# Kernel optimization log

Hardware: AMD Instinct MI355X
Metric: run time of the kernel (lower is better)

Reference implementation:

```python
import jax, jax.numpy as jnp
import numpy as np

B, T, EMB, NDIM = 8, 2048, 1024, 1024


def setup_inputs() -> dict:
    key = jax.random.key(0)
    k1, k2, k3, k4 = jax.random.split(key, 4)
    X = jax.random.normal(k1, (B, T, EMB), dtype=jnp.float32)
    # Linear(emb, ndim, bias=False); stored as [emb, ndim] so projection is X @ W.
    scale = 1.0 / np.sqrt(EMB)
    Wq = jax.random.normal(k2, (EMB, NDIM), dtype=jnp.float32) * scale
    Wk = jax.random.normal(k3, (EMB, NDIM), dtype=jnp.float32) * scale
    Wv = jax.random.normal(k4, (EMB, NDIM), dtype=jnp.float32) * scale
    return {"X": X, "Wq": Wq, "Wk": Wk, "Wv": Wv}


def reference(X, Wq, Wk, Wv):
    ndim = Wq.shape[-1]
    T_ = X.shape[1]
    Q = X @ Wq  # [B,T,ndim]
    K = X @ Wk  # [B,T,ndim]
    V = X @ Wv  # [B,T,ndim]
    # scores[b,t,s] = Q[b,t] . K[b,s], scaled by ndim^-0.5
    scores = jnp.einsum("btd,bsd->bts", Q, K) * (ndim ** -0.5)
    mask = jnp.tril(jnp.ones((T_, T_), dtype=bool))  # causal lower-triangular
    scores = jnp.where(mask, scores, -jnp.inf)
    # NOTE: source uses F.softmax(..., dim=1) -> normalize over the QUERY axis
    # (columns of the [T,T] matrix), not the usual key axis. Replicated faithfully.
    probs = jax.nn.softmax(scores, axis=1)
    # dropout is identity in eval / p=0 deterministic baseline
    return probs @ V  # [B,T,ndim]
```

## Files before the change

kernel.cpp:

```cpp
#include <hip/hip_runtime.h>
#include <hip/hip_bf16.h>

#define B_   8
#define T_   2048
#define EMB_ 1024
#define ND_  1024
#define NTB  16
#define NPAIR 136

typedef __attribute__((ext_vector_type(8))) short   bf8_t;
typedef __attribute__((ext_vector_type(4))) float   f32x4;

__device__ __forceinline__ unsigned short f2bf(float f) {
  union { float f; unsigned int u; } c; c.f = f;
  unsigned int u = c.u;
  unsigned int r = (u + 0x7FFFu + ((u >> 16) & 1u)) >> 16;
  return (unsigned short)r;
}

__device__ __forceinline__ float bf2f(unsigned short b) {
  union { unsigned int u; float f; } c; c.u = ((unsigned int)b) << 16;
  return c.f;
}

__device__ __forceinline__ void gload_lds16(const unsigned short* g, unsigned short* l) {
  __builtin_amdgcn_global_load_lds(
      (const __attribute__((address_space(1))) unsigned int*)g,
      (__attribute__((address_space(3))) unsigned int*)l,
      16, 0, 0);
}

__device__ __forceinline__ void stage128x32(const unsigned short* __restrict__ g,
                                            int lda, unsigned short* lds,
                                            int wave, int lane) {
  const int rsub = lane >> 2;
  const int koff = (lane & 3) * 8;
#pragma unroll
  for (int c = 0; c < 2; ++c) {
    const int chunk = wave * 2 + c;
    const unsigned short* src = g + (size_t)(chunk * 16 + rsub) * lda + koff;
    gload_lds16(src, lds + chunk * 512);
  }
}

__device__ __forceinline__ void mfma_step(const unsigned short* As, const unsigned short* Bs,
                                          f32x4 acc[4][4], int lane, int wm, int wn) {
  const int r = lane & 15, k8 = (lane >> 4) * 8;
  bf8_t a[4], b[4];
#pragma unroll
  for (int m = 0; m < 4; ++m)
    a[m] = *(const bf8_t*)(As + (size_t)(wm * 64 + m * 16 + r) * 32 + k8);
#pragma unroll
  for (int n = 0; n < 4; ++n)
    b[n] = *(const bf8_t*)(Bs + (size_t)(wn * 64 + n * 16 + r) * 32 + k8);
#pragma unroll
  for (int m = 0; m < 4; ++m)
#pragma unroll
    for (int n = 0; n < 4; ++n)
      acc[m][n] = __builtin_amdgcn_mfma_f32_16x16x32_bf16(a[m], b[n], acc[m][n], 0, 0, 0);
}

__device__ __forceinline__ void zero_acc(f32x4 acc[4][4]) {
#pragma unroll
  for (int m = 0; m < 4; ++m)
#pragma unroll
    for (int n = 0; n < 4; ++n)
#pragma unroll
      for (int q = 0; q < 4; ++q) acc[m][n][q] = 0.f;
}

__device__ __forceinline__ void tri_decode(int p, int& tblk, int& sblk) {
  int t = (int)((sqrtf(8.0f * (float)p + 1.0f) - 1.0f) * 0.5f);
  while ((t + 1) * (t + 2) / 2 <= p) ++t;
  while (t * (t + 1) / 2 > p) --t;
  tblk = t;
  sblk = p - t * (t + 1) / 2;
}

__global__ void __launch_bounds__(256) cvt_x_kernel(const float* __restrict__ in,
                                                    unsigned short* __restrict__ out) {
  const int i = (blockIdx.x * 256 + threadIdx.x) * 4;
  float4 v = *(const float4*)(in + i);
  ushort4 o = make_ushort4(f2bf(v.x), f2bf(v.y), f2bf(v.z), f2bf(v.w));
  *(ushort4*)(out + i) = o;
}

__global__ void __launch_bounds__(256) transpose_w_kernel(const float* __restrict__ W,
                                                          unsigned short* __restrict__ Wt,
                                                          float cscale) {
  __shared__ unsigned short tile[32][33];
  const int n0 = blockIdx.x * 32, k0 = blockIdx.y * 32;
  const int tx = threadIdx.x & 31, ty = threadIdx.x >> 5;
#pragma unroll
  for (int r = 0; r < 32; r += 8) {
    float v = W[(size_t)(k0 + ty + r) * ND_ + n0 + tx];
    tile[tx][ty + r] = f2bf(v * cscale);
  }
  __syncthreads();
#pragma unroll
  for (int r = 0; r < 32; r += 8) {
    Wt[(size_t)(n0 + ty + r) * EMB_ + k0 + tx] = tile[ty + r][tx];
  }
}


#define LDSA(d, h) (lds256 + ((d) * 2 + (h)) * 8192)
#define LDSB(d, h) (lds256 + 32768 + ((d) * 2 + (h)) * 8192)
#define SB0() __builtin_amdgcn_sched_barrier(0)
#define BAR() __builtin_amdgcn_s_barrier()

__device__ __forceinline__ void stage_half(const unsigned short* __restrict__ g, int lda,
                                           unsigned short* lhalf, int wave, int lane) {
  const int r3 = lane >> 3, c3 = lane & 7;
  const int colsw = ((c3 ^ r3) << 3);
#pragma unroll
  for (int j = 0; j < 2; ++j) {
    const int row = wave * 8 + r3 + 64 * j;
    gload_lds16(g + (size_t)row * lda + colsw, lhalf + wave * 512 + j * 4096);
  }
}

__device__ __forceinline__ bf8_t read_frag(const unsigned short* half, int r, int ks, int lane) {
  const int col = (((ks) << 5) + ((lane >> 4) << 3)) ^ ((r & 7) << 3);
  return *(const bf8_t*)(half + r * 64 + col);
}

#define MFMA_QUAD(MB, AF, AOFF) do { \
  __builtin_amdgcn_s_setprio(1); \
  _Pragma("unroll") \
  for (int mi = 0; mi < 2; ++mi) \
    _Pragma("unroll") \
    for (int nf = 0; nf < 4; ++nf) \
      _Pragma("unroll") \
      for (int ks = 0; ks < 2; ++ks) \
        acc[(MB) * 2 + mi][nf] = __builtin_amdgcn_mfma_f32_16x16x32_bf16( \
            (AF)[(AOFF) + mi][ks], bfr[nf][ks], acc[(MB) * 2 + mi][nf], 0, 0, 0); \
  __builtin_amdgcn_s_setprio(0); \
} while (0)

template <int OUTMODE>
__global__ void __launch_bounds__(512, 2)
gemm_xw256_kernel(const unsigned short* __restrict__ A,
                  const unsigned short* __restrict__ Bt,
                  unsigned short* __restrict__ C) {
  extern __shared__ unsigned short lds256[];
  const int tid = threadIdx.x, lane = tid & 63, wave = tid >> 6;
  const int wm = wave >> 2, wn = wave & 3;
  const int m0 = blockIdx.y * 256, n0 = blockIdx.x * 256;
  const unsigned short* Ab = A + (size_t)m0 * EMB_;
  const unsigned short* Bb = Bt + (size_t)n0 * EMB_;

  f32x4 acc[8][4];
#pragma unroll
  for (int i = 0; i < 8; ++i)
#pragma unroll
    for (int j = 0; j < 4; ++j)
#pragma unroll
      for (int q = 0; q < 4; ++q) acc[i][j][q] = 0.f;

  const int arow = lane & 15;
  const int brow = (wn & 1) * 64 + (lane & 15);

  stage_half(Ab,                            EMB_, LDSA(0, 0), wave, lane);
  stage_half(Ab + (size_t)128 * EMB_,       EMB_, LDSA(0, 1), wave, lane);
  stage_half(Bb,                            EMB_, LDSB(0, 0), wave, lane);
  stage_half(Bb + (size_t)128 * EMB_,       EMB_, LDSB(0, 1), wave, lane);
  stage_half(Bb + 64,                       EMB_, LDSB(1, 0), wave, lane);
  stage_half(Bb + (size_t)128 * EMB_ + 64,  EMB_, LDSB(1, 1), wave, lane);
  stage_half(Ab + 64,                       EMB_, LDSA(1, 0), wave, lane);
  asm volatile("s_waitcnt vmcnt(6)" ::: "memory");
  SB0(); BAR(); SB0();

  for (int t = 0; t < 16; ++t) {
    const int d = t & 1;
    const unsigned short* Ah = LDSA(d, wm);
    const unsigned short* Bh = LDSB(d, wn >> 1);

    bf8_t bfr[4][2], af[4][2];
#pragma unroll
    for (int nf = 0; nf < 4; ++nf)
#pragma unroll
      for (int ks = 0; ks < 2; ++ks) bfr[nf][ks] = read_frag(Bh, brow + nf * 16, ks, lane);
#pragma unroll
    for (int mf = 0; mf < 4; ++mf)
#pragma unroll
      for (int ks = 0; ks < 2; ++ks) af[mf][ks] = read_frag(Ah, arow + mf * 16, ks, lane);
    SB0();
    if (t < 15) stage_half(Ab + (size_t)128 * EMB_ + (size_t)(t + 1) * 64, EMB_, LDSA(d ^ 1, 1), wave, lane);
    SB0(); BAR(); SB0();
    MFMA_QUAD(0, af, 0);
    SB0();
    asm volatile("s_waitcnt lgkmcnt(0)" ::: "memory");
    SB0(); BAR(); SB0();

    if (t < 14) stage_half(Bb + (size_t)(t + 2) * 64, EMB_, LDSB(d, 0), wave, lane);
    SB0(); BAR(); SB0();
    MFMA_QUAD(1, af, 2);
    SB0(); BAR(); SB0();

    bf8_t af2[4][2];
#pragma unroll
    for (int mf = 0; mf < 4; ++mf)
#pragma unroll
      for (int ks = 0; ks < 2; ++ks) af2[mf][ks] = read_frag(Ah, arow + (mf + 4) * 16, ks, lane);
    SB0();
    if (t < 14) stage_half(Bb + (size_t)128 * EMB_ + (size_t)(t + 2) * 64, EMB_, LDSB(d, 1), wave, lane);
    SB0(); BAR(); SB0();
    MFMA_QUAD(2, af2, 0);
    SB0();
    asm volatile("s_waitcnt lgkmcnt(0)" ::: "memory");
    SB0(); BAR(); SB0();

    if (t < 14) stage_half(Ab + (size_t)(t + 2) * 64, EMB_, LDSA(d, 0), wave, lane);
    if (t < 14)      { asm volatile("s_waitcnt vmcnt(6)" ::: "memory"); }
    else if (t == 14){ asm volatile("s_waitcnt vmcnt(0)" ::: "memory"); }
    SB0(); BAR(); SB0();
    MFMA_QUAD(3, af2, 2);
    SB0(); BAR(); SB0();
  }

  const int cc = lane & 15, cr4 = (lane >> 4) << 2;
#pragma unroll
  for (int mf = 0; mf < 8; ++mf)
#pragma unroll
    for (int nf = 0; nf < 4; ++nf)
#pragma unroll
      for (int q = 0; q < 4; ++q) {
        const int row = m0 + wm * 128 + mf * 16 + cr4 + q;
        const int col = n0 + wn * 64 + nf * 16 + cc;
        const unsigned short val = f2bf(acc[mf][nf][q]);
        if (OUTMODE == 0) {
          C[(size_t)row * ND_ + col] = val;
        } else {
          const int bb = row >> 11, tt = row & 2047;
          C[((size_t)bb * ND_ + col) * T_ + tt] = val;
        }
      }
}

__global__ void __launch_bounds__(256) scoretile_kernel(const unsigned short* __restrict__ Qb,
                                                        const unsigned short* __restrict__ Kb,
                                                        unsigned short* __restrict__ Sb,
                                                        float* __restrict__ pm,
                                                        float* __restrict__ pl) {
  int tblk, sblk;
  tri_decode(blockIdx.x, tblk, sblk);
  const int b = blockIdx.y;
  __shared__ unsigned short As[128 * 32], Bs[128 * 32];
  __shared__ float redm[2][2][4][16], redl[2][2][4][16];
  const int tid = threadIdx.x, lane = tid & 63, wave = tid >> 6;
  const int wm = wave >> 1, wn = wave & 1;
  const int t0 = tblk * 128, s0 = sblk * 128;
  const unsigned short* Qbase = Qb + ((size_t)b * T_ + t0) * ND_;
  const unsigned short* Kbase = Kb + ((size_t)b * T_ + s0) * ND_;
  f32x4 acc[4][4];
  zero_acc(acc);
  for (int k = 0; k < ND_; k += 32) {
    __syncthreads();
    stage128x32(Qbase + k, ND_, As, wave, lane);
    stage128x32(Kbase + k, ND_, Bs, wave, lane);
    __syncthreads();
    mfma_step(As, Bs, acc, lane, wm, wn);
  }
  const int cr = ((lane >> 4) << 2), cc = lane & 15;
  unsigned short* Pbase = Sb + (size_t)b * T_ * T_;
  const bool diag = (tblk == sblk);
  float rm[4], rl[4];
#pragma unroll
  for (int n = 0; n < 4; ++n) { rm[n] = -1e30f; rl[n] = 0.f; }
#pragma unroll
  for (int n = 0; n < 4; ++n) {
    const int s = s0 + wn * 64 + n * 16 + cc;
#pragma unroll
    for (int m = 0; m < 4; ++m)
#pragma unroll
      for (int q = 0; q < 4; ++q) {
        const int t = t0 + wm * 64 + m * 16 + cr + q;
        if (!diag || t >= s) {
          const unsigned short bv = f2bf(acc[m][n][q]);
          Pbase[(size_t)t * T_ + s] = bv;
          const float v = bf2f(bv);
          const float mm = fmaxf(rm[n], v);
          rl[n] = rl[n] * __expf(rm[n] - mm) + __expf(v - mm);
          rm[n] = mm;
        }
      }
  }
#pragma unroll
  for (int n = 0; n < 4; ++n) {
#pragma unroll
    for (int off = 16; off < 64; off <<= 1) {
      const float om = __shfl_xor(rm[n], off);
      const float ol = __shfl_xor(rl[n], off);
      const float mm = fmaxf(rm[n], om);
      rl[n] = rl[n] * __expf(rm[n] - mm) + ol * __expf(om - mm);
      rm[n] = mm;
    }
  }
  __syncthreads();
  if (lane < 16) {
#pragma unroll
    for (int n = 0; n < 4; ++n) { redm[wm][wn][n][lane] = rm[n]; redl[wm][wn][n][lane] = rl[n]; }
  }
  __syncthreads();
  if (wm == 0 && lane < 16) {
    const size_t base = (((size_t)b * NTB + sblk) * NTB + tblk) * 128;
#pragma unroll
    for (int n = 0; n < 4; ++n) {
      const float m0v = redm[0][wn][n][lane], l0v = redl[0][wn][n][lane];
      const float m1v = redm[1][wn][n][lane], l1v = redl[1][wn][n][lane];
      const float mm = fmaxf(m0v, m1v);
      const float ll = l0v * __expf(m0v - mm) + l1v * __expf(m1v - mm);
      pm[base + wn * 64 + n * 16 + lane] = mm;
      pl[base + wn * 64 + n * 16 + lane] = ll;
    }
  }
}

__global__ void __launch_bounds__(128) colreduce_kernel(const float* __restrict__ pm,
                                                        const float* __restrict__ pl,
                                                        float* __restrict__ colmax,
                                                        float* __restrict__ colinv) {
  const int sblk = blockIdx.x, b = blockIdx.y, c = threadIdx.x;
  float m = -1e30f, l = 0.f;
  for (int tblk = sblk; tblk < NTB; ++tblk) {
    const size_t base = (((size_t)b * NTB + sblk) * NTB + tblk) * 128;
    const float om = pm[base + c], ol = pl[base + c];
    const float mm = fmaxf(m, om);
    l = l * __expf(m - mm) + ol * __expf(om - mm);
    m = mm;
  }
  colmax[(size_t)b * T_ + sblk * 128 + c] = m;
  colinv[(size_t)b * T_ + sblk * 128 + c] = 1.0f / l;
}

__global__ void __launch_bounds__(256) pscale_kernel(unsigned short* __restrict__ Pb,
                                                     const float* __restrict__ colmax,
                                                     const float* __restrict__ colinv) {
  int tblk, sblk;
  tri_decode(blockIdx.x, tblk, sblk);
  const int b = blockIdx.y;
  const int s0 = sblk * 128, t0 = tblk * 128;
  const int tid = threadIdx.x;
  const int col8 = (tid & 15) * 8;
  const int rbase = tid >> 4;
  unsigned short* Pbase = Pb + (size_t)b * T_ * T_;
  float ms[8], inv[8];
#pragma unroll
  for (int j = 0; j < 8; ++j) {
    ms[j]  = colmax[(size_t)b * T_ + s0 + col8 + j];
    inv[j] = colinv[(size_t)b * T_ + s0 + col8 + j];
  }
  const bool diag = (tblk == sblk);
  for (int r = rbase; r < 128; r += 16) {
    const int t = t0 + r;
    unsigned short* p = Pbase + (size_t)t * T_ + s0 + col8;
    bf8_t v = *(bf8_t*)p;
#pragma unroll
    for (int j = 0; j < 8; ++j) {
      float pv = 0.f;
      if (!diag || t >= s0 + col8 + j) {
        pv = __expf(bf2f((unsigned short)v[j]) - ms[j]) * inv[j];
      }
      v[j] = (short)f2bf(pv);
    }
    *(bf8_t*)p = v;
  }
}

__global__ void __launch_bounds__(256) gemm_pv_kernel(const unsigned short* __restrict__ Pb,
                                                      const unsigned short* __restrict__ Vt,
                                                      float* __restrict__ out) {
  __shared__ unsigned short As[128 * 32], Bs[128 * 32];
  const int nblk = blockIdx.x, tblk = blockIdx.y, b = blockIdx.z;
  const int tid = threadIdx.x, lane = tid & 63, wave = tid >> 6;
  const int wm = wave >> 1, wn = wave & 1;
  const int m0 = tblk * 128, n0 = nblk * 128;
  const unsigned short* Ab = Pb + (size_t)b * T_ * T_ + (size_t)m0 * T_;
  const unsigned short* Bb = Vt + (size_t)b * ND_ * T_ + (size_t)n0 * T_;
  f32x4 acc[4][4];
  zero_acc(acc);
  const int kmax = m0 + 128;
  for (int k = 0; k < kmax; k += 32) {
    __syncthreads();
    stage128x32(Ab + k, T_, As, wave, lane);
    stage128x32(Bb + k, T_, Bs, wave, lane);
    __syncthreads();
    mfma_step(As, Bs, acc, lane, wm, wn);
  }
  float* Cb = out + (size_t)b * T_ * ND_;
  const int cr = ((lane >> 4) << 2), cc = lane & 15;
#pragma unroll
  for (int m = 0; m < 4; ++m)
#pragma unroll
    for (int n = 0; n < 4; ++n)
#pragma unroll
      for (int q = 0; q < 4; ++q) {
        const int row = m0 + wm * 64 + m * 16 + cr + q;
        const int col = n0 + wn * 64 + n * 16 + cc;
        Cb[(size_t)row * ND_ + col] = acc[m][n][q];
      }
}

extern "C" void kernel_launch(void* const* d_in, const int* in_sizes, int n_in,
                              void* d_out, int out_size, void* d_ws, size_t ws_size,
                              hipStream_t stream) {
  const float* X  = (const float*)d_in[0];
  const float* Wq = (const float*)d_in[1];
  const float* Wk = (const float*)d_in[2];
  const float* Wv = (const float*)d_in[3];
  float* out = (float*)d_out;
  (void)in_sizes; (void)n_in; (void)out_size;

  char* ws = (char*)d_ws;
  size_t off = 0;
  auto alloc = [&](size_t bytes) {
    void* p = ws + off;
    off += (bytes + 255) & ~(size_t)255;
    return p;
  };
  unsigned short* Xb  = (unsigned short*)alloc((size_t)B_ * T_ * EMB_ * 2);
  unsigned short* Wtq = (unsigned short*)alloc((size_t)ND_ * EMB_ * 2);
  unsigned short* Wtk = (unsigned short*)alloc((size_t)ND_ * EMB_ * 2);
  unsigned short* Wtv = (unsigned short*)alloc((size_t)ND_ * EMB_ * 2);
  unsigned short* Qb  = (unsigned short*)alloc((size_t)B_ * T_ * ND_ * 2);
  unsigned short* Kb  = (unsigned short*)alloc((size_t)B_ * T_ * ND_ * 2);
  unsigned short* Vt  = (unsigned short*)alloc((size_t)B_ * ND_ * T_ * 2);
  float* colmax = (float*)alloc((size_t)B_ * T_ * 4);
  float* colinv = (float*)alloc((size_t)B_ * T_ * 4);
  float* pm     = (float*)alloc((size_t)B_ * NTB * NTB * 128 * 4);
  float* pl     = (float*)alloc((size_t)B_ * NTB * NTB * 128 * 4);
  unsigned short* Pb  = (unsigned short*)alloc((size_t)B_ * T_ * T_ * 2);
  if (off > ws_size) return;

  hipFuncSetAttribute((const void*)&gemm_xw256_kernel<0>,
                      hipFuncAttributeMaxDynamicSharedMemorySize, 131072);
  hipFuncSetAttribute((const void*)&gemm_xw256_kernel<1>,
                      hipFuncAttributeMaxDynamicSharedMemorySize, 131072);

  hipLaunchKernelGGL(cvt_x_kernel, dim3((B_ * T_ * EMB_) / 1024), dim3(256), 0, stream, X, Xb);
  hipLaunchKernelGGL(transpose_w_kernel, dim3(32, 32), dim3(256), 0, stream, Wq, Wtq, 0.03125f);
  hipLaunchKernelGGL(transpose_w_kernel, dim3(32, 32), dim3(256), 0, stream, Wk, Wtk, 1.0f);
  hipLaunchKernelGGL(transpose_w_kernel, dim3(32, 32), dim3(256), 0, stream, Wv, Wtv, 1.0f);
  hipLaunchKernelGGL((gemm_xw256_kernel<0>), dim3(ND_ / 256, (B_ * T_) / 256), dim3(512), 131072, stream, Xb, Wtq, Qb);
  hipLaunchKernelGGL((gemm_xw256_kernel<0>), dim3(ND_ / 256, (B_ * T_) / 256), dim3(512), 131072, stream, Xb, Wtk, Kb);
  hipLaunchKernelGGL((gemm_xw256_kernel<1>), dim3(ND_ / 256, (B_ * T_) / 256), dim3(512), 131072, stream, Xb, Wtv, Vt);
  hipLaunchKernelGGL(scoretile_kernel, dim3(NPAIR, B_), dim3(256), 0, stream, Qb, Kb, Pb, pm, pl);
  hipLaunchKernelGGL(colreduce_kernel, dim3(NTB, B_), dim3(128), 0, stream, pm, pl, colmax, colinv);
  hipLaunchKernelGGL(pscale_kernel, dim3(NPAIR, B_), dim3(256), 0, stream, Pb, colmax, colinv);
  hipLaunchKernelGGL(gemm_pv_kernel, dim3(ND_ / 128, T_ / 128, B_), dim3(256), 0, stream, Pb, Vt, out);
}
```

Baseline: 328.1 us.

## Move score and PV GEMMs onto 256-tile pipelined MFMA path with balanced pairing

Replaces the simple 128x128 score-tile and PV GEMM kernels with versions built on the tuned 256-wide, 8-wave, double-buffered, swizzled-LDS pipeline already used for the projections. The score kernel now covers 256x256 causal tiles (36 pairs per batch) and writes explicit zeros above the diagonal. The PV kernel gives each block two row blocks, tb and 15-tb, so every block does a similar amount of causal work. The intent is higher MFMA utilisation and less per-tile load overhead, at the cost of more masked work on diagonal tiles and fewer, larger blocks.

New measurement: 305.2 us. -7.0%, faster.

```diff
diff --git a/kernel.cpp b/kernel.cpp
--- a/kernel.cpp
+++ b/kernel.cpp
@@ -7,6 +7,8 @@
 #define ND_  1024
 #define NTB  16
 #define NPAIR 136
+#define NTB2 8
+#define NPAIR2 36
 
 typedef __attribute__((ext_vector_type(8))) short   bf8_t;
 typedef __attribute__((ext_vector_type(4))) float   f32x4;
@@ -28,45 +30,6 @@
       (const __attribute__((address_space(1))) unsigned int*)g,
       (__attribute__((address_space(3))) unsigned int*)l,
       16, 0, 0);
-}
-
-__device__ __forceinline__ void stage128x32(const unsigned short* __restrict__ g,
-                                            int lda, unsigned short* lds,
-                                            int wave, int lane) {
-  const int rsub = lane >> 2;
-  const int koff = (lane & 3) * 8;
-#pragma unroll
-  for (int c = 0; c < 2; ++c) {
-    const int chunk = wave * 2 + c;
-    const unsigned short* src = g + (size_t)(chunk * 16 + rsub) * lda + koff;
-    gload_lds16(src, lds + chunk * 512);
-  }
-}
-
-__device__ __forceinline__ void mfma_step(const unsigned short* As, const unsigned short* Bs,
-                                          f32x4 acc[4][4], int lane, int wm, int wn) {
-  const int r = lane & 15, k8 = (lane >> 4) * 8;
-  bf8_t a[4], b[4];
-#pragma unroll
-  for (int m = 0; m < 4; ++m)
-    a[m] = *(const bf8_t*)(As + (size_t)(wm * 64 + m * 16 + r) * 32 + k8);
-#pragma unroll
-  for (int n = 0; n < 4; ++n)
-    b[n] = *(const bf8_t*)(Bs + (size_t)(wn * 64 + n * 16 + r) * 32 + k8);
-#pragma unroll
-  for (int m = 0; m < 4; ++m)
-#pragma unroll
-    for (int n = 0; n < 4; ++n)
-      acc[m][n] = __builtin_amdgcn_mfma_f32_16x16x32_bf16(a[m], b[n], acc[m][n], 0, 0, 0);
-}
-
-__device__ __forceinline__ void zero_acc(f32x4 acc[4][4]) {
-#pragma unroll
-  for (int m = 0; m < 4; ++m)
-#pragma unroll
-    for (int n = 0; n < 4; ++n)
-#pragma unroll
-      for (int q = 0; q < 4; ++q) acc[m][n][q] = 0.f;
 }
 
 __device__ __forceinline__ void tri_decode(int p, int& tblk, int& sblk) {
@@ -77,6 +40,25 @@
   sblk = p - t * (t + 1) / 2;
 }
 
+#define SB0() __builtin_amdgcn_sched_barrier(0)
+#define BAR() __builtin_amdgcn_s_barrier()
+
+__device__ __forceinline__ void stage_half(const unsigned short* __restrict__ g, int lda,
+                                           unsigned short* lhalf, int wave, int lane) {
+  const int r3 = lane >> 3, c3 = lane & 7;
+  const int colsw = ((c3 ^ r3) << 3);
+#pragma unroll
+  for (int j = 0; j < 2; ++j) {
+    const int row = wave * 8 + r3 + 64 * j;
+    gload_lds16(g + (size_t)row * lda + colsw, lhalf + wave * 512 + j * 4096);
+  }
+}
+
+__device__ __forceinline__ bf8_t read_frag(const unsigned short* half, int r, int ks, int lane) {
+  const int col = (((ks) << 5) + ((lane >> 4) << 3)) ^ ((r & 7) << 3);
+  return *(const bf8_t*)(half + r * 64 + col);
+}
+
 __global__ void __launch_bounds__(256) cvt_x_kernel(const float* __restrict__ in,
                                                     unsigned short* __restrict__ out) {
   const int i = (blockIdx.x * 256 + threadIdx.x) * 4;
@@ -103,27 +85,8 @@
   }
 }
 
-
 #define LDSA(d, h) (lds256 + ((d) * 2 + (h)) * 8192)
 #define LDSB(d, h) (lds256 + 32768 + ((d) * 2 + (h)) * 8192)
-#define SB0() __builtin_amdgcn_sched_barrier(0)
-#define BAR() __builtin_amdgcn_s_barrier()
-
-__device__ __forceinline__ void stage_half(const unsigned short* __restrict__ g, int lda,
-                                           unsigned short* lhalf, int wave, int lane) {
-  const int r3 = lane >> 3, c3 = lane & 7;
-  const int colsw = ((c3 ^ r3) << 3);
-#pragma unroll
-  for (int j = 0; j < 2; ++j) {
-    const int row = wave * 8 + r3 + 64 * j;
-    gload_lds16(g + (size_t)row * lda + colsw, lhalf + wave * 512 + j * 4096);
-  }
-}
-
-__device__ __forceinline__ bf8_t read_frag(const unsigned short* half, int r, int ks, int lane) {
-  const int col = (((ks) << 5) + ((lane >> 4) << 3)) ^ ((r & 7) << 3);
-  return *(const bf8_t*)(half + r * 64 + col);
-}
 
 #define MFMA_QUAD(MB, AF, AOFF) do { \
   __builtin_amdgcn_s_setprio(1); \
@@ -138,6 +101,60 @@
   __builtin_amdgcn_s_setprio(0); \
 } while (0)
 
+#define GEMM256_LOOP(ABASE, BBASE, LDK) \
+  stage_half((ABASE),                           (LDK), LDSA(0, 0), wave, lane); \
+  stage_half((ABASE) + (size_t)128 * (LDK),     (LDK), LDSA(0, 1), wave, lane); \
+  stage_half((BBASE),                           (LDK), LDSB(0, 0), wave, lane); \
+  stage_half((BBASE) + (size_t)128 * (LDK),     (LDK), LDSB(0, 1), wave, lane); \
+  stage_half((BBASE) + 64,                      (LDK), LDSB(1, 0), wave, lane); \
+  stage_half((BBASE) + (size_t)128 * (LDK) + 64,(LDK), LDSB(1, 1), wave, lane); \
+  stage_half((ABASE) + 64,                      (LDK), LDSA(1, 0), wave, lane); \
+  asm volatile("s_waitcnt vmcnt(6)" ::: "memory"); \
+  SB0(); BAR(); SB0(); \
+  for (int t = 0; t < 16; ++t) { \
+    const int d = t & 1; \
+    const unsigned short* Ah = LDSA(d, wm); \
+    const unsigned short* Bh = LDSB(d, wn >> 1); \
+    bf8_t bfr[4][2], af[4][2]; \
+    _Pragma("unroll") \
+    for (int nf = 0; nf < 4; ++nf) \
+      _Pragma("unroll") \
+      for (int ks = 0; ks < 2; ++ks) bfr[nf][ks] = read_frag(Bh, brow + nf * 16, ks, lane); \
+    _Pragma("unroll") \
+    for (int mf = 0; mf < 4; ++mf) \
+      _Pragma("unroll") \
+      for (int ks = 0; ks < 2; ++ks) af[mf][ks] = read_frag(Ah, arow + mf * 16, ks, lane); \
+    SB0(); \
+    if (t < 15) stage_half((ABASE) + (size_t)128 * (LDK) + (size_t)(t + 1) * 64, (LDK), LDSA(d ^ 1, 1), wave, lane); \
+    SB0(); BAR(); SB0(); \
+    MFMA_QUAD(0, af, 0); \
+    SB0(); \
+    asm volatile("s_waitcnt lgkmcnt(0)" ::: "memory"); \
+    SB0(); BAR(); SB0(); \
+    if (t < 14) stage_half((BBASE) + (size_t)(t + 2) * 64, (LDK), LDSB(d, 0), wave, lane); \
+    SB0(); BAR(); SB0(); \
+    MFMA_QUAD(1, af, 2); \
+    SB0(); BAR(); SB0(); \
+    bf8_t af2[4][2]; \
+    _Pragma("unroll") \
+    for (int mf = 0; mf < 4; ++mf) \
+      _Pragma("unroll") \
+      for (int ks = 0; ks < 2; ++ks) af2[mf][ks] = read_frag(Ah, arow + (mf + 4) * 16, ks, lane); \
+    SB0(); \
+    if (t < 14) stage_half((BBASE) + (size_t)128 * (LDK) + (size_t)(t + 2) * 64, (LDK), LDSB(d, 1), wave, lane); \
+    SB0(); BAR(); SB0(); \
+    MFMA_QUAD(2, af2, 0); \
+    SB0(); \
+    asm volatile("s_waitcnt lgkmcnt(0)" ::: "memory"); \
+    SB0(); BAR(); SB0(); \
+    if (t < 14) stage_half((ABASE) + (size_t)(t + 2) * 64, (LDK), LDSA(d, 0), wave, lane); \
+    if (t < 14)      { asm volatile("s_waitcnt vmcnt(6)" ::: "memory"); } \
+    else if (t == 14){ asm volatile("s_waitcnt vmcnt(0)" ::: "memory"); } \
+    SB0(); BAR(); SB0(); \
+    MFMA_QUAD(3, af2, 2); \
+    SB0(); BAR(); SB0(); \
+  }
+
 template <int OUTMODE>
 __global__ void __launch_bounds__(512, 2)
 gemm_xw256_kernel(const unsigned short* __restrict__ A,
@@ -149,7 +166,6 @@
   const int m0 = blockIdx.y * 256, n0 = blockIdx.x * 256;
   const unsigned short* Ab = A + (size_t)m0 * EMB_;
   const unsigned short* Bb = Bt + (size_t)n0 * EMB_;
-
   f32x4 acc[8][4];
 #pragma unroll
   for (int i = 0; i < 8; ++i)
@@ -157,67 +173,10 @@
     for (int j = 0; j < 4; ++j)
 #pragma unroll
       for (int q = 0; q < 4; ++q) acc[i][j][q] = 0.f;
-
   const int arow = lane & 15;
   const int brow = (wn & 1) * 64 + (lane & 15);
 
-  stage_half(Ab,                            EMB_, LDSA(0, 0), wave, lane);
-  stage_half(Ab + (size_t)128 * EMB_,       EMB_, LDSA(0, 1), wave, lane);
-  stage_half(Bb,                            EMB_, LDSB(0, 0), wave, lane);
-  stage_half(Bb + (size_t)128 * EMB_,       EMB_, LDSB(0, 1), wave, lane);
-  stage_half(Bb + 64,                       EMB_, LDSB(1, 0), wave, lane);
-  stage_half(Bb + (size_t)128 * EMB_ + 64,  EMB_, LDSB(1, 1), wave, lane);
-  stage_half(Ab + 64,                       EMB_, LDSA(1, 0), wave, lane);
-  asm volatile("s_waitcnt vmcnt(6)" ::: "memory");
-  SB0(); BAR(); SB0();
-
-  for (int t = 0; t < 16; ++t) {
-    const int d = t & 1;
-    const unsigned short* Ah = LDSA(d, wm);
-    const unsigned short* Bh = LDSB(d, wn >> 1);
-
-    bf8_t bfr[4][2], af[4][2];
-#pragma unroll
-    for (int nf = 0; nf < 4; ++nf)
-#pragma unroll
-      for (int ks = 0; ks < 2; ++ks) bfr[nf][ks] = read_frag(Bh, brow + nf * 16, ks, lane);
-#pragma unroll
-    for (int mf = 0; mf < 4; ++mf)
-#pragma unroll
-      for (int ks = 0; ks < 2; ++ks) af[mf][ks] = read_frag(Ah, arow + mf * 16, ks, lane);
-    SB0();
-    if (t < 15) stage_half(Ab + (size_t)128 * EMB_ + (size_t)(t + 1) * 64, EMB_, LDSA(d ^ 1, 1), wave, lane);
-    SB0(); BAR(); SB0();
-    MFMA_QUAD(0, af, 0);
-    SB0();
-    asm volatile("s_waitcnt lgkmcnt(0)" ::: "memory");
-    SB0(); BAR(); SB0();
-
-    if (t < 14) stage_half(Bb + (size_t)(t + 2) * 64, EMB_, LDSB(d, 0), wave, lane);
-    SB0(); BAR(); SB0();
-    MFMA_QUAD(1, af, 2);
-    SB0(); BAR(); SB0();
-
-    bf8_t af2[4][2];
-#pragma unroll
-    for (int mf = 0; mf < 4; ++mf)
-#pragma unroll
-      for (int ks = 0; ks < 2; ++ks) af2[mf][ks] = read_frag(Ah, arow + (mf + 4) * 16, ks, lane);
-    SB0();
-    if (t < 14) stage_half(Bb + (size_t)128 * EMB_ + (size_t)(t + 2) * 64, EMB_, LDSB(d, 1), wave, lane);
-    SB0(); BAR(); SB0();
-    MFMA_QUAD(2, af2, 0);
-    SB0();
-    asm volatile("s_waitcnt lgkmcnt(0)" ::: "memory");
-    SB0(); BAR(); SB0();
-
-    if (t < 14) stage_half(Ab + (size_t)(t + 2) * 64, EMB_, LDSA(d, 0), wave, lane);
-    if (t < 14)      { asm volatile("s_waitcnt vmcnt(6)" ::: "memory"); }
-    else if (t == 14){ asm volatile("s_waitcnt vmcnt(0)" ::: "memory"); }
-    SB0(); BAR(); SB0();
-    MFMA_QUAD(3, af2, 2);
-    SB0(); BAR(); SB0();
-  }
+  GEMM256_LOOP(Ab, Bb, EMB_)
 
   const int cc = lane & 15, cr4 = (lane >> 4) << 2;
 #pragma unroll
@@ -238,100 +197,109 @@
       }
 }
 
-__global__ void __launch_bounds__(256) scoretile_kernel(const unsigned short* __restrict__ Qb,
-                                                        const unsigned short* __restrict__ Kb,
-                                                        unsigned short* __restrict__ Sb,
-                                                        float* __restrict__ pm,
-                                                        float* __restrict__ pl) {
-  int tblk, sblk;
-  tri_decode(blockIdx.x, tblk, sblk);
+__global__ void __launch_bounds__(512, 2)
+scoretile256_kernel(const unsigned short* __restrict__ Qb,
+                    const unsigned short* __restrict__ Kb,
+                    unsigned short* __restrict__ Sb,
+                    float* __restrict__ pm,
+                    float* __restrict__ pl) {
+  extern __shared__ unsigned short lds256[];
+  int tr, sr;
+  tri_decode(blockIdx.x, tr, sr);
   const int b = blockIdx.y;
-  __shared__ unsigned short As[128 * 32], Bs[128 * 32];
-  __shared__ float redm[2][2][4][16], redl[2][2][4][16];
   const int tid = threadIdx.x, lane = tid & 63, wave = tid >> 6;
-  const int wm = wave >> 1, wn = wave & 1;
-  const int t0 = tblk * 128, s0 = sblk * 128;
-  const unsigned short* Qbase = Qb + ((size_t)b * T_ + t0) * ND_;
-  const unsigned short* Kbase = Kb + ((size_t)b * T_ + s0) * ND_;
-  f32x4 acc[4][4];
-  zero_acc(acc);
-  for (int k = 0; k < ND_; k += 32) {
-    __syncthreads();
-    stage128x32(Qbase + k, ND_, As, wave, lane);
-    stage128x32(Kbase + k, ND_, Bs, wave, lane);
-    __syncthreads();
-    mfma_step(As, Bs, acc, lane, wm, wn);
-  }
-  const int cr = ((lane >> 4) << 2), cc = lane & 15;
-  unsigned short* Pbase = Sb + (size_t)b * T_ * T_;
-  const bool diag = (tblk == sblk);
+  const int wm = wave >> 2, wn = wave & 3;
+  const int t0 = tr * 256, s0 = sr * 256;
+  const unsigned short* Ab = Qb + ((size_t)b * T_ + t0) * ND_;
+  const unsigned short* Bb = Kb + ((size_t)b * T_ + s0) * ND_;
+  f32x4 acc[8][4];
+#pragma unroll
+  for (int i = 0; i < 8; ++i)
+#pragma unroll
+    for (int j = 0; j < 4; ++j)
+#pragma unroll
+      for (int q = 0; q < 4; ++q) acc[i][j][q] = 0.f;
+  const int arow = lane & 15;
+  const int brow = (wn & 1) * 64 + (lane & 15);
+
+  GEMM256_LOOP(Ab, Bb, ND_)
+
+  const int cc = lane & 15, cr4 = (lane >> 4) << 2;
+  const bool diag = (tr == sr);
+  unsigned short* Sbase = Sb + (size_t)b * T_ * T_;
   float rm[4], rl[4];
 #pragma unroll
-  for (int n = 0; n < 4; ++n) { rm[n] = -1e30f; rl[n] = 0.f; }
-#pragma unroll
-  for (int n = 0; n < 4; ++n) {
-    const int s = s0 + wn * 64 + n * 16 + cc;
-#pragma unroll
-    for (int m = 0; m < 4; ++m)
+  for (int nf = 0; nf < 4; ++nf) { rm[nf] = -1e30f; rl[nf] = 0.f; }
+#pragma unroll
+  for (int mf = 0; mf < 8; ++mf)
+#pragma unroll
+    for (int nf = 0; nf < 4; ++nf)
 #pragma unroll
       for (int q = 0; q < 4; ++q) {
-        const int t = t0 + wm * 64 + m * 16 + cr + q;
-        if (!diag || t >= s) {
-          const unsigned short bv = f2bf(acc[m][n][q]);
-          Pbase[(size_t)t * T_ + s] = bv;
+        const int t = t0 + wm * 128 + mf * 16 + cr4 + q;
+        const int s = s0 + wn * 64 + nf * 16 + cc;
+        const bool ok = !diag || (t >= s);
+        const unsigned short bv = ok ? f2bf(acc[mf][nf][q]) : (unsigned short)0;
+        Sbase[(size_t)t * T_ + s] = bv;
+        if (ok) {
           const float v = bf2f(bv);
-          const float mm = fmaxf(rm[n], v);
-          rl[n] = rl[n] * __expf(rm[n] - mm) + __expf(v - mm);
-          rm[n] = mm;
+          const float mm = fmaxf(rm[nf], v);
+          rl[nf] = rl[nf] * __expf(rm[nf] - mm) + __expf(v - mm);
+          rm[nf] = mm;
         }
       }
-  }
-#pragma unroll
-  for (int n = 0; n < 4; ++n) {
+#pragma unroll
+  for (int nf = 0; nf < 4; ++nf) {
 #pragma unroll
     for (int off = 16; off < 64; off <<= 1) {
-      const float om = __shfl_xor(rm[n], off);
-      const float ol = __shfl_xor(rl[n], off);
-      const float mm = fmaxf(rm[n], om);
-      rl[n] = rl[n] * __expf(rm[n] - mm) + ol * __expf(om - mm);
-      rm[n] = mm;
+      const float om = __shfl_xor(rm[nf], off);
+      const float ol = __shfl_xor(rl[nf], off);
+      const float mm = fmaxf(rm[nf], om);
+      rl[nf] = rl[nf] * __expf(rm[nf] - mm) + ol * __expf(om - mm);
+      rm[nf] = mm;
     }
   }
   __syncthreads();
+  float* red = (float*)lds256;
   if (lane < 16) {
 #pragma unroll
-    for (int n = 0; n < 4; ++n) { redm[wm][wn][n][lane] = rm[n]; redl[wm][wn][n][lane] = rl[n]; }
+    for (int nf = 0; nf < 4; ++nf) {
+      red[((wm * 4 + wn) * 4 + nf) * 16 + lane] = rm[nf];
+      red[512 + ((wm * 4 + wn) * 4 + nf) * 16 + lane] = rl[nf];
+    }
   }
   __syncthreads();
   if (wm == 0 && lane < 16) {
-    const size_t base = (((size_t)b * NTB + sblk) * NTB + tblk) * 128;
-#pragma unroll
-    for (int n = 0; n < 4; ++n) {
-      const float m0v = redm[0][wn][n][lane], l0v = redl[0][wn][n][lane];
-      const float m1v = redm[1][wn][n][lane], l1v = redl[1][wn][n][lane];
+    const size_t base = (((size_t)b * NTB2 + sr) * NTB2 + tr) * 256;
+#pragma unroll
+    for (int nf = 0; nf < 4; ++nf) {
+      const float m0v = red[((0 * 4 + wn) * 4 + nf) * 16 + lane];
+      const float l0v = red[512 + ((0 * 4 + wn) * 4 + nf) * 16 + lane];
+      const float m1v = red[((1 * 4 + wn) * 4 + nf) * 16 + lane];
+      const float l1v = red[512 + ((1 * 4 + wn) * 4 + nf) * 16 + lane];
       const float mm = fmaxf(m0v, m1v);
       const float ll = l0v * __expf(m0v - mm) + l1v * __expf(m1v - mm);
-      pm[base + wn * 64 + n * 16 + lane] = mm;
-      pl[base + wn * 64 + n * 16 + lane] = ll;
+      pm[base + wn * 64 + nf * 16 + lane] = mm;
+      pl[base + wn * 64 + nf * 16 + lane] = ll;
     }
   }
 }
 
-__global__ void __launch_bounds__(128) colreduce_kernel(const float* __restrict__ pm,
+__global__ void __launch_bounds__(256) colreduce_kernel(const float* __restrict__ pm,
                                                         const float* __restrict__ pl,
                                                         float* __restrict__ colmax,
                                                         float* __restrict__ colinv) {
-  const int sblk = blockIdx.x, b = blockIdx.y, c = threadIdx.x;
+  const int sr = blockIdx.x, b = blockIdx.y, c = threadIdx.x;
   float m = -1e30f, l = 0.f;
-  for (int tblk = sblk; tblk < NTB; ++tblk) {
-    const size_t base = (((size_t)b * NTB + sblk) * NTB + tblk) * 128;
+  for (int tr = sr; tr < NTB2; ++tr) {
+    const size_t base = (((size_t)b * NTB2 + sr) * NTB2 + tr) * 256;
     const float om = pm[base + c], ol = pl[base + c];
     const float mm = fmaxf(m, om);
     l = l * __expf(m - mm) + ol * __expf(om - mm);
     m = mm;
   }
-  colmax[(size_t)b * T_ + sblk * 128 + c] = m;
-  colinv[(size_t)b * T_ + sblk * 128 + c] = 1.0f / l;
+  colmax[(size_t)b * T_ + sr * 256 + c] = m;
+  colinv[(size_t)b * T_ + sr * 256 + c] = 1.0f / l;
 }
 
 __global__ void __launch_bounds__(256) pscale_kernel(unsigned short* __restrict__ Pb,
@@ -368,38 +336,109 @@
   }
 }
 
-__global__ void __launch_bounds__(256) gemm_pv_kernel(const unsigned short* __restrict__ Pb,
-                                                      const unsigned short* __restrict__ Vt,
-                                                      float* __restrict__ out) {
-  __shared__ unsigned short As[128 * 32], Bs[128 * 32];
-  const int nblk = blockIdx.x, tblk = blockIdx.y, b = blockIdx.z;
+#define MFMA_Q8(MB) do { \
+  __builtin_amdgcn_s_setprio(1); \
+  _Pragma("unroll") \
+  for (int nf = 0; nf < 4; ++nf) \
+    _Pragma("unroll") \
+    for (int ks = 0; ks < 2; ++ks) \
+      acc[(MB)][nf] = __builtin_amdgcn_mfma_f32_16x16x32_bf16( \
+          af[(MB)][ks], bfr[nf][ks], acc[(MB)][nf], 0, 0, 0); \
+  __builtin_amdgcn_s_setprio(0); \
+} while (0)
+
+__device__ __forceinline__ void pv_segment(const unsigned short* __restrict__ Ab,
+                                           const unsigned short* __restrict__ Bb,
+                                           float* __restrict__ Cb,
+                                           int ktiles, unsigned short* lds256,
+                                           int lane, int wave) {
+  const int wm = wave >> 2, wn = wave & 3;
+  const int arow = lane & 15;
+  f32x4 acc[4][4];
+#pragma unroll
+  for (int i = 0; i < 4; ++i)
+#pragma unroll
+    for (int j = 0; j < 4; ++j)
+#pragma unroll
+      for (int q = 0; q < 4; ++q) acc[i][j][q] = 0.f;
+
+  stage_half(Ab,                           T_, lds256,                     wave, lane);
+  stage_half(Bb,                           T_, lds256 + 16384,             wave, lane);
+  stage_half(Bb + (size_t)128 * T_,        T_, lds256 + 16384 + 8192,      wave, lane);
+  stage_half(Ab + 64,                      T_, lds256 + 8192,              wave, lane);
+  stage_half(Bb + 64,                      T_, lds256 + 16384 + 2 * 8192,  wave, lane);
+  stage_half(Bb + (size_t)128 * T_ + 64,   T_, lds256 + 16384 + 3 * 8192,  wave, lane);
+  asm volatile("s_waitcnt vmcnt(6)" ::: "memory");
+  SB0(); BAR(); SB0();
+
+  for (int t = 0; t < ktiles; ++t) {
+    const int d = t & 1;
+    const unsigned short* Ah = lds256 + d * 8192;
+    const unsigned short* Bh = lds256 + 16384 + (d * 2 + (wn >> 1)) * 8192;
+    bf8_t bfr[4][2], af[4][2];
+#pragma unroll
+    for (int nf = 0; nf < 4; ++nf)
+#pragma unroll
+      for (int ks = 0; ks < 2; ++ks)
+        bfr[nf][ks] = read_frag(Bh, (wn & 1) * 64 + nf * 16 + arow, ks, lane);
+#pragma unroll
+    for (int mf = 0; mf < 4; ++mf)
+#pragma unroll
+      for (int ks = 0; ks < 2; ++ks)
+        af[mf][ks] = read_frag(Ah, wm * 64 + mf * 16 + arow, ks, lane);
+    SB0(); BAR(); SB0();
+    MFMA_Q8(0);
+    SB0();
+    asm volatile("s_waitcnt lgkmcnt(0)" ::: "memory");
+    SB0(); BAR(); SB0();
+    if (t < ktiles - 2) stage_half(Ab + (size_t)(t + 2) * 64, T_, lds256 + d * 8192, wave, lane);
+    SB0(); BAR(); SB0();
+    MFMA_Q8(1);
+    SB0(); BAR(); SB0();
+    if (t < ktiles - 2) stage_half(Bb + (size_t)(t + 2) * 64, T_, lds256 + 16384 + (d * 2) * 8192, wave, lane);
+    SB0(); BAR(); SB0();
+    MFMA_Q8(2);
+    SB0(); BAR(); SB0();
+    if (t < ktiles - 2) stage_half(Bb + (size_t)128 * T_ + (size_t)(t + 2) * 64, T_, lds256 + 16384 + (d * 2 + 1) * 8192, wave, lane);
+    if (t < ktiles - 2)      { asm volatile("s_waitcnt vmcnt(6)" ::: "memory"); }
+    else if (t == ktiles - 2){ asm volatile("s_waitcnt vmcnt(0)" ::: "memory"); }
+    SB0(); BAR(); SB0();
+    MFMA_Q8(3);
+    SB0(); BAR(); SB0();
+  }
+
+  const int cc = lane & 15, cr4 = (lane >> 4) << 2;
+#pragma unroll
+  for (int mf = 0; mf < 4; ++mf)
+#pragma unroll
+    for (int nf = 0; nf < 4; ++nf)
+#pragma unroll
+      for (int q = 0; q < 4; ++q) {
+        const int row = wm * 64 + mf * 16 + cr4 + q;
+        const int col = wn * 64 + nf * 16 + cc;
+        Cb[(size_t)row * ND_ + col] = acc[mf][nf][q];
+      }
+}
+
+__global__ void __launch_bounds__(512, 2)
+gemm_pv256_kernel(const unsigned short* __restrict__ Pb,
+                  const unsigned short* __restrict__ Vt,
+                  float* __restrict__ out) {
+  extern __shared__ unsigned short lds256[];
+  const int pair = blockIdx.x;
+  const int ncol = blockIdx.y;
+  const int b = blockIdx.z;
   const int tid = threadIdx.x, lane = tid & 63, wave = tid >> 6;
-  const int wm = wave >> 1, wn = wave & 1;
-  const int m0 = tblk * 128, n0 = nblk * 128;
-  const unsigned short* Ab = Pb + (size_t)b * T_ * T_ + (size_t)m0 * T_;
-  const unsigned short* Bb = Vt + (size_t)b * ND_ * T_ + (size_t)n0 * T_;
-  f32x4 acc[4][4];
-  zero_acc(acc);
-  const int kmax = m0 + 128;
-  for (int k = 0; k < kmax; k += 32) {
-    __syncthreads();
-    stage128x32(Ab + k, T_, As, wave, lane);
-    stage128x32(Bb + k, T_, Bs, wave, lane);
-    __syncthreads();
-    mfma_step(As, Bs, acc, lane, wm, wn);
-  }
-  float* Cb = out + (size_t)b * T_ * ND_;
-  const int cr = ((lane >> 4) << 2), cc = lane & 15;
-#pragma unroll
-  for (int m = 0; m < 4; ++m)
-#pragma unroll
-    for (int n = 0; n < 4; ++n)
-#pragma unroll
-      for (int q = 0; q < 4; ++q) {
-        const int row = m0 + wm * 64 + m * 16 + cr + q;
-        const int col = n0 + wn * 64 + n * 16 + cc;
-        Cb[(size_t)row * ND_ + col] = acc[m][n][q];
-      }
+  const int tbs[2] = {pair, 15 - pair};
+#pragma unroll
+  for (int si = 0; si < 2; ++si) {
+    const int tb = tbs[si];
+    const int ktiles = 2 * tb + 2;
+    pv_segment(Pb + (size_t)b * T_ * T_ + (size_t)tb * 128 * T_,
+               Vt + (size_t)b * ND_ * T_ + (size_t)ncol * 256 * T_,
+               out + (size_t)b * T_ * ND_ + (size_t)tb * 128 * ND_ + ncol * 256,
+               ktiles, lds256, lane, wave);
+  }
 }
 
 extern "C" void kernel_launch(void* const* d_in, const int* in_sizes, int n_in,
@@ -428,8 +467,8 @@
   unsigned short* Vt  = (unsigned short*)alloc((size_t)B_ * ND_ * T_ * 2);
   float* colmax = (float*)alloc((size_t)B_ * T_ * 4);
   float* colinv = (float*)alloc((size_t)B_ * T_ * 4);
-  float* pm     = (float*)alloc((size_t)B_ * NTB * NTB * 128 * 4);
-  float* pl     = (float*)alloc((size_t)B_ * NTB * NTB * 128 * 4);
+  float* pm     = (float*)alloc((size_t)B_ * NTB2 * NTB2 * 256 * 4);
+  float* pl     = (float*)alloc((size_t)B_ * NTB2 * NTB2 * 256 * 4);
   unsigned short* Pb  = (unsigned short*)alloc((size_t)B_ * T_ * T_ * 2);
   if (off > ws_size) return;
 
@@ -437,6 +476,10 @@
                       hipFuncAttributeMaxDynamicSharedMemorySize, 131072);
   hipFuncSetAttribute((const void*)&gemm_xw256_kernel<1>,
                       hipFuncAttributeMaxDynamicSharedMemorySize, 131072);
+  hipFuncSetAttribute((const void*)&scoretile256_kernel,
+                      hipFuncAttributeMaxDynamicSharedMemorySize, 131072);
+  hipFuncSetAttribute((const void*)&gemm_pv256_kernel,
+                      hipFuncAttributeMaxDynamicSharedMemorySize, 98304);
 
   hipLaunchKernelGGL(cvt_x_kernel, dim3((B_ * T_ * EMB_) / 1024), dim3(256), 0, stream, X, Xb);
   hipLaunchKernelGGL(transpose_w_kernel, dim3(32, 32), dim3(256), 0, stream, Wq, Wtq, 0.03125f);
@@ -445,8 +488,8 @@
   hipLaunchKernelGGL((gemm_xw256_kernel<0>), dim3(ND_ / 256, (B_ * T_) / 256), dim3(512), 131072, stream, Xb, Wtq, Qb);
   hipLaunchKernelGGL((gemm_xw256_kernel<0>), dim3(ND_ / 256, (B_ * T_) / 256), dim3(512), 131072, stream, Xb, Wtk, Kb);
   hipLaunchKernelGGL((gemm_xw256_kernel<1>), dim3(ND_ / 256, (B_ * T_) / 256), dim3(512), 131072, stream, Xb, Wtv, Vt);
-  hipLaunchKernelGGL(scoretile_kernel, dim3(NPAIR, B_), dim3(256), 0, stream, Qb, Kb, Pb, pm, pl);
-  hipLaunchKernelGGL(colreduce_kernel, dim3(NTB, B_), dim3(128), 0, stream, pm, pl, colmax, colinv);
+  hipLaunchKernelGGL(scoretile256_kernel, dim3(NPAIR2, B_), dim3(512), 131072, stream, Qb, Kb, Pb, pm, pl);
+  hipLaunchKernelGGL(colreduce_kernel, dim3(NTB2, B_), dim3(256), 0, stream, pm, pl, colmax, colinv);
   hipLaunchKernelGGL(pscale_kernel, dim3(NPAIR, B_), dim3(256), 0, stream, Pb, colmax, colinv);
-  hipLaunchKernelGGL(gemm_pv_kernel, dim3(ND_ / 128, T_ / 128, B_), dim3(256), 0, stream, Pb, Vt, out);
-}
+  hipLaunchKernelGGL(gemm_pv256_kernel, dim3(NTB2, ND_ / 256, B_), dim3(512), 98304, stream, Pb, Vt, out);
+}
```
